# Kernel tuning notes

Hardware: AMD Instinct MI355X
Metric: run time of the kernel (lower is better)

The kernel has to match this reference:

```python
import jax, jax.numpy as jnp
import numpy as np

B, N, D, E = 16, 4096, 1024, 64
TOP_K = 2
ROUTING_FLOOR_BASE = 0.05
CAP_LOW, CAP_HIGH, T_MAX = 0.5, 0.6, 1000


def setup_inputs() -> dict:
    key = jax.random.key(0)
    k1, k2, k3 = jax.random.split(key, 3)
    tokens_B = jax.random.normal(k1, (B, N, D), dtype=jnp.float32)
    t = jax.random.randint(k2, (B,), 0, T_MAX, dtype=jnp.int32)
    W_g = jax.random.normal(k3, (E, D), dtype=jnp.float32) * (1.0 / np.sqrt(D))
    b_g = jnp.zeros((E,), dtype=jnp.float32)
    return {"tokens_B": tokens_B, "t": t, "W_g": W_g, "b_g": b_g}


def _apply_routing_floor(probs, floor):
    # interpolate toward uniform so each expert gets >= floor mass
    e = probs.shape[-1]
    if floor <= 0.0:
        return probs
    alpha = min(floor * e, 1.0)
    return (1.0 - alpha) * probs + alpha / e


def _hard_cap(probs, t):
    # cap(t) = cap_low + (cap_high + cap_low) * t/T_max  (faithful to source)
    t_norm = t.astype(probs.dtype) / T_MAX
    cap = (CAP_LOW + (CAP_HIGH + CAP_LOW) * t_norm)[:, None, None]  # (B,1,1)
    excess = jax.nn.relu(probs - cap)
    capped = probs - excess
    headroom = jax.nn.relu(cap - capped)
    headroom_sum = jnp.clip(headroom.sum(-1, keepdims=True), 1e-8)
    capped = capped + excess.sum(-1, keepdims=True) * (headroom / headroom_sum)
    # torch version runs under no_grad; use straight-through so gate still trains
    return probs + jax.lax.stop_gradient(capped - probs)


def _topk_mask(probs, k):
    vals, idx = jax.lax.top_k(probs, k)  # (B,N,k)
    onehot = jax.nn.one_hot(idx, probs.shape[-1], dtype=probs.dtype)  # (B,N,k,E)
    return jnp.einsum('bnk,bnke->bne', vals, onehot)


def reference(tokens_B, t, W_g, b_g):
    logits = jnp.einsum('bnd,ed->bne', tokens_B, W_g) + b_g  # (B,N,E)
    probs = jax.nn.softmax(logits, axis=-1)
    floor = min(ROUTING_FLOOR_BASE, 0.15 / max(E, 1))
    probs = _apply_routing_floor(probs, floor)
    capped = _hard_cap(probs, t)
    gates = _topk_mask(capped, TOP_K)  # sparse gate mask (B,N,E)
    return gates
```

## Files before the change

### kernel.cpp

```cpp
#include <hip/hip_runtime.h>
#include <hip/hip_bf16.h>

typedef __attribute__((ext_vector_type(8))) short short8;
typedef __attribute__((ext_vector_type(4))) short sh4;
typedef __attribute__((ext_vector_type(4))) float floatx4;

__device__ __forceinline__ bool better(float va, int ia, float vb, int ib) {
    return (va > vb) || (va == vb && ia < ib);
}
__device__ __forceinline__ bool betterd(double va, int ia, double vb, int ib) {
    return (va > vb) || (va == vb && ia < ib);
}

__device__ __forceinline__ short bf16_rn(float f) {
    __hip_bfloat16 h = __float2bfloat16(f);
    return *reinterpret_cast<short*>(&h);
}
__device__ __forceinline__ float bf16_up(short s) {
    return __uint_as_float(((unsigned)(unsigned short)s) << 16);
}

__device__ __forceinline__ void split8(float4 a, float4 b, short8& hi, short8& lo) {
    float v[8] = {a.x, a.y, a.z, a.w, b.x, b.y, b.z, b.w};
    #pragma unroll
    for (int i = 0; i < 8; ++i) {
        short h = bf16_rn(v[i]);
        hi[i] = h;
        lo[i] = bf16_rn(v[i] - bf16_up(h));
    }
}

#define MFMA(A, B, C) __builtin_amdgcn_mfma_f32_16x16x32_bf16((A), (B), (C), 0, 0, 0)

__global__ __launch_bounds__(256)
void wsplit_kernel(const float* __restrict__ Wg,
                   short* __restrict__ whi,
                   short* __restrict__ wlo)
{
    const int i = blockIdx.x * 256 + threadIdx.x;
    float4 v = reinterpret_cast<const float4*>(Wg)[i];
    float vv[4] = {v.x, v.y, v.z, v.w};
    sh4 h, l;
    #pragma unroll
    for (int j = 0; j < 4; ++j) {
        short hh = bf16_rn(vv[j]);
        h[j] = hh;
        l[j] = bf16_rn(vv[j] - bf16_up(hh));
    }
    reinterpret_cast<sh4*>(whi)[i] = h;
    reinterpret_cast<sh4*>(wlo)[i] = l;
}

__global__ __launch_bounds__(256, 4)
void router_kernel(const float* __restrict__ tokens,
                   const int* __restrict__ tarr,
                   const float* __restrict__ bg,
                   float* __restrict__ out,
                   int* __restrict__ flagCount,
                   int* __restrict__ flagList,
                   int listCap,
                   const short* __restrict__ whi,
                   const short* __restrict__ wlo)
{
    __shared__ __align__(16) float gtile[64 * 64];

    const int lane = threadIdx.x & 63;
    const int wave = threadIdx.x >> 6;
    const int c16  = lane & 15;
    const int quad = lane >> 4;

    const int tokenBase = blockIdx.x * 64;
    const int token     = tokenBase + wave * 16 + c16;

    const float4* ap = reinterpret_cast<const float4*>(tokens) + (size_t)token * 256 + quad * 2;
    const short8* whiV = reinterpret_cast<const short8*>(whi);
    const short8* wloV = reinterpret_cast<const short8*>(wlo);
    const int w0 = (c16 +  0) * 128 + quad;
    const int w1 = (c16 + 16) * 128 + quad;
    const int w2 = (c16 + 32) * 128 + quad;
    const int w3 = (c16 + 48) * 128 + quad;

    floatx4 acc0 = {0.f, 0.f, 0.f, 0.f};
    floatx4 acc1 = acc0, acc2 = acc0, acc3 = acc0;

    #pragma unroll
    for (int kb = 0; kb < 32; ++kb) {
        float4 a0 = ap[kb * 8];
        float4 a1 = ap[kb * 8 + 1];
        short8 h0 = whiV[w0 + kb * 4];
        short8 h1 = whiV[w1 + kb * 4];
        short8 h2 = whiV[w2 + kb * 4];
        short8 h3 = whiV[w3 + kb * 4];
        short8 l0 = wloV[w0 + kb * 4];
        short8 l1 = wloV[w1 + kb * 4];
        short8 l2 = wloV[w2 + kb * 4];
        short8 l3 = wloV[w3 + kb * 4];

        short8 ahi, alo;
        split8(a0, a1, ahi, alo);

        acc0 = MFMA(ahi, h0, acc0); acc0 = MFMA(alo, h0, acc0); acc0 = MFMA(ahi, l0, acc0);
        acc1 = MFMA(ahi, h1, acc1); acc1 = MFMA(alo, h1, acc1); acc1 = MFMA(ahi, l1, acc1);
        acc2 = MFMA(ahi, h2, acc2); acc2 = MFMA(alo, h2, acc2); acc2 = MFMA(ahi, l2, acc2);
        acc3 = MFMA(ahi, h3, acc3); acc3 = MFMA(alo, h3, acc3); acc3 = MFMA(ahi, l3, acc3);
    }

    const float b0f = bg[c16 +  0];
    const float b1f = bg[c16 + 16];
    const float b2f = bg[c16 + 32];
    const float b3f = bg[c16 + 48];

    const float tb  = (float)tarr[tokenBase >> 12];
    const float cap = 0.5f + 1.1f * (tb / 1000.0f);

    const float A1 = 0.85f;
    const float A2 = 0.15f / 64.0f;

    #pragma unroll
    for (int r = 0; r < 4; ++r) {
        float l0 = acc0[r] + b0f;
        float l1 = acc1[r] + b1f;
        float l2 = acc2[r] + b2f;
        float l3 = acc3[r] + b3f;

        float mx = fmaxf(fmaxf(l0, l1), fmaxf(l2, l3));
        #pragma unroll
        for (int off = 8; off >= 1; off >>= 1)
            mx = fmaxf(mx, __shfl_xor(mx, off));

        float e0 = expf(l0 - mx), e1 = expf(l1 - mx);
        float e2 = expf(l2 - mx), e3 = expf(l3 - mx);
        float s = e0 + e1 + e2 + e3;
        #pragma unroll
        for (int off = 8; off >= 1; off >>= 1)
            s += __shfl_xor(s, off);
        float inv = 1.0f / s;

        float p0 = A1 * (e0 * inv) + A2;
        float p1 = A1 * (e1 * inv) + A2;
        float p2 = A1 * (e2 * inv) + A2;
        float p3 = A1 * (e3 * inv) + A2;

        float x0 = fmaxf(p0 - cap, 0.f), x1 = fmaxf(p1 - cap, 0.f);
        float x2 = fmaxf(p2 - cap, 0.f), x3 = fmaxf(p3 - cap, 0.f);
        float m0 = p0 - x0, m1 = p1 - x1, m2 = p2 - x2, m3 = p3 - x3;
        float h0 = fmaxf(cap - m0, 0.f), h1 = fmaxf(cap - m1, 0.f);
        float h2 = fmaxf(cap - m2, 0.f), h3 = fmaxf(cap - m3, 0.f);
        float sx = x0 + x1 + x2 + x3;
        float sh = h0 + h1 + h2 + h3;
        #pragma unroll
        for (int off = 8; off >= 1; off >>= 1) {
            sx += __shfl_xor(sx, off);
            sh += __shfl_xor(sh, off);
        }
        sh = fmaxf(sh, 1e-8f);
        float sc = sx / sh;
        float c0 = m0 + sc * h0;
        float c1 = m1 + sc * h1;
        float c2 = m2 + sc * h2;
        float c3 = m3 + sc * h3;

        const int iA = c16, iB = c16 + 16, iC = c16 + 32, iD = c16 + 48;
        float v1, v2; int j1, j2;
        if (better(c0, iA, c1, iB)) { v1 = c0; j1 = iA; v2 = c1; j2 = iB; }
        else                        { v1 = c1; j1 = iB; v2 = c0; j2 = iA; }
        if (better(c2, iC, v1, j1))      { v2 = v1; j2 = j1; v1 = c2; j1 = iC; }
        else if (better(c2, iC, v2, j2)) { v2 = c2; j2 = iC; }
        if (better(c3, iD, v1, j1))      { v2 = v1; j2 = j1; v1 = c3; j1 = iD; }
        else if (better(c3, iD, v2, j2)) { v2 = c3; j2 = iD; }

        #pragma unroll
        for (int off = 1; off < 16; off <<= 1) {
            float w1 = __shfl_xor(v1, off); int k1 = __shfl_xor(j1, off);
            float w2 = __shfl_xor(v2, off); int k2 = __shfl_xor(j2, off);
            if (better(w1, k1, v1, j1)) {
                if (better(v1, j1, w2, k2)) { v2 = v1; j2 = j1; }
                else                        { v2 = w2; j2 = k2; }
                v1 = w1; j1 = k1;
            } else if (better(w1, k1, v2, j2)) {
                v2 = w1; j2 = k1;
            }
        }

        float g0 = (iA == j1 || iA == j2) ? c0 : 0.f;
        float g1 = (iB == j1 || iB == j2) ? c1 : 0.f;
        float g2 = (iC == j1 || iC == j2) ? c2 : 0.f;
        float g3 = (iD == j1 || iD == j2) ? c3 : 0.f;

        float t0 = (iA == j1 || iA == j2) ? -3.0e38f : c0;
        float t1 = (iB == j1 || iB == j2) ? -3.0e38f : c1;
        float t2 = (iC == j1 || iC == j2) ? -3.0e38f : c2;
        float t3 = (iD == j1 || iD == j2) ? -3.0e38f : c3;
        float m3v = fmaxf(fmaxf(t0, t1), fmaxf(t2, t3));
        #pragma unroll
        for (int off = 8; off >= 1; off >>= 1)
            m3v = fmaxf(m3v, __shfl_xor(m3v, off));

        const int tl = wave * 16 + quad * 4 + r;
        bool flag = ((v2 - m3v) < 1e-4f) || (sx > 0.0f);
        if (flag && c16 == 0) {
            int pos = atomicAdd(flagCount, 1);
            if (pos < listCap) flagList[pos] = tokenBase + tl;
        }

        gtile[tl * 64 + iA] = g0;
        gtile[tl * 64 + iB] = g1;
        gtile[tl * 64 + iC] = g2;
        gtile[tl * 64 + iD] = g3;
    }

    __syncthreads();

    const uint4* src = reinterpret_cast<const uint4*>(gtile);
    uint4* dst = reinterpret_cast<uint4*>(out + (size_t)tokenBase * 64);
    dst[threadIdx.x]       = src[threadIdx.x];
    dst[threadIdx.x + 256] = src[threadIdx.x + 256];
    dst[threadIdx.x + 512] = src[threadIdx.x + 512];
    dst[threadIdx.x + 768] = src[threadIdx.x + 768];
}

__global__ __launch_bounds__(256, 4)
void router_kernel_legacy(const float* __restrict__ tokens,
                          const int* __restrict__ tarr,
                          const float* __restrict__ Wg,
                          const float* __restrict__ bg,
                          float* __restrict__ out,
                          int* __restrict__ flagCount,
                          int* __restrict__ flagList,
                          int listCap)
{
    __shared__ __align__(16) float gtile[64 * 64];

    const int lane = threadIdx.x & 63;
    const int wave = threadIdx.x >> 6;
    const int c16  = lane & 15;
    const int quad = lane >> 4;

    const int tokenBase = blockIdx.x * 64;
    const int token     = tokenBase + wave * 16 + c16;

    const float4* ap = reinterpret_cast<const float4*>(tokens) + (size_t)token * 256 + quad * 2;
    const float4* wp0 = reinterpret_cast<const float4*>(Wg) + (size_t)(c16 +  0) * 256 + quad * 2;
    const float4* wp1 = reinterpret_cast<const float4*>(Wg) + (size_t)(c16 + 16) * 256 + quad * 2;
    const float4* wp2 = reinterpret_cast<const float4*>(Wg) + (size_t)(c16 + 32) * 256 + quad * 2;
    const float4* wp3 = reinterpret_cast<const float4*>(Wg) + (size_t)(c16 + 48) * 256 + quad * 2;

    floatx4 acc0 = {0.f, 0.f, 0.f, 0.f};
    floatx4 acc1 = acc0, acc2 = acc0, acc3 = acc0;

    for (int kb = 0; kb < 32; ++kb) {
        short8 ahi, alo;
        split8(ap[kb * 8], ap[kb * 8 + 1], ahi, alo);
        {
            short8 whi, wlo;
            split8(wp0[kb * 8], wp0[kb * 8 + 1], whi, wlo);
            acc0 = MFMA(ahi, whi, acc0);
            acc0 = MFMA(alo, whi, acc0);
            acc0 = MFMA(ahi, wlo, acc0);
        }
        {
            short8 whi, wlo;
            split8(wp1[kb * 8], wp1[kb * 8 + 1], whi, wlo);
            acc1 = MFMA(ahi, whi, acc1);
            acc1 = MFMA(alo, whi, acc1);
            acc1 = MFMA(ahi, wlo, acc1);
        }
        {
            short8 whi, wlo;
            split8(wp2[kb * 8], wp2[kb * 8 + 1], whi, wlo);
            acc2 = MFMA(ahi, whi, acc2);
            acc2 = MFMA(alo, whi, acc2);
            acc2 = MFMA(ahi, wlo, acc2);
        }
        {
            short8 whi, wlo;
            split8(wp3[kb * 8], wp3[kb * 8 + 1], whi, wlo);
            acc3 = MFMA(ahi, whi, acc3);
            acc3 = MFMA(alo, whi, acc3);
            acc3 = MFMA(ahi, wlo, acc3);
        }
    }

    const float b0f = bg[c16 +  0];
    const float b1f = bg[c16 + 16];
    const float b2f = bg[c16 + 32];
    const float b3f = bg[c16 + 48];

    const float tb  = (float)tarr[tokenBase >> 12];
    const float cap = 0.5f + 1.1f * (tb / 1000.0f);

    const float A1 = 0.85f;
    const float A2 = 0.15f / 64.0f;

    #pragma unroll
    for (int r = 0; r < 4; ++r) {
        float l0 = acc0[r] + b0f;
        float l1 = acc1[r] + b1f;
        float l2 = acc2[r] + b2f;
        float l3 = acc3[r] + b3f;

        float mx = fmaxf(fmaxf(l0, l1), fmaxf(l2, l3));
        #pragma unroll
        for (int off = 8; off >= 1; off >>= 1)
            mx = fmaxf(mx, __shfl_xor(mx, off));

        float e0 = expf(l0 - mx), e1 = expf(l1 - mx);
        float e2 = expf(l2 - mx), e3 = expf(l3 - mx);
        float s = e0 + e1 + e2 + e3;
        #pragma unroll
        for (int off = 8; off >= 1; off >>= 1)
            s += __shfl_xor(s, off);
        float inv = 1.0f / s;

        float p0 = A1 * (e0 * inv) + A2;
        float p1 = A1 * (e1 * inv) + A2;
        float p2 = A1 * (e2 * inv) + A2;
        float p3 = A1 * (e3 * inv) + A2;

        float x0 = fmaxf(p0 - cap, 0.f), x1 = fmaxf(p1 - cap, 0.f);
        float x2 = fmaxf(p2 - cap, 0.f), x3 = fmaxf(p3 - cap, 0.f);
        float m0 = p0 - x0, m1 = p1 - x1, m2 = p2 - x2, m3 = p3 - x3;
        float h0 = fmaxf(cap - m0, 0.f), h1 = fmaxf(cap - m1, 0.f);
        float h2 = fmaxf(cap - m2, 0.f), h3 = fmaxf(cap - m3, 0.f);
        float sx = x0 + x1 + x2 + x3;
        float sh = h0 + h1 + h2 + h3;
        #pragma unroll
        for (int off = 8; off >= 1; off >>= 1) {
            sx += __shfl_xor(sx, off);
            sh += __shfl_xor(sh, off);
        }
        sh = fmaxf(sh, 1e-8f);
        float sc = sx / sh;
        float c0 = m0 + sc * h0;
        float c1 = m1 + sc * h1;
        float c2 = m2 + sc * h2;
        float c3 = m3 + sc * h3;

        const int iA = c16, iB = c16 + 16, iC = c16 + 32, iD = c16 + 48;
        float v1, v2; int j1, j2;
        if (better(c0, iA, c1, iB)) { v1 = c0; j1 = iA; v2 = c1; j2 = iB; }
        else                        { v1 = c1; j1 = iB; v2 = c0; j2 = iA; }
        if (better(c2, iC, v1, j1))      { v2 = v1; j2 = j1; v1 = c2; j1 = iC; }
        else if (better(c2, iC, v2, j2)) { v2 = c2; j2 = iC; }
        if (better(c3, iD, v1, j1))      { v2 = v1; j2 = j1; v1 = c3; j1 = iD; }
        else if (better(c3, iD, v2, j2)) { v2 = c3; j2 = iD; }

        #pragma unroll
        for (int off = 1; off < 16; off <<= 1) {
            float w1 = __shfl_xor(v1, off); int k1 = __shfl_xor(j1, off);
            float w2 = __shfl_xor(v2, off); int k2 = __shfl_xor(j2, off);
            if (better(w1, k1, v1, j1)) {
                if (better(v1, j1, w2, k2)) { v2 = v1; j2 = j1; }
                else                        { v2 = w2; j2 = k2; }
                v1 = w1; j1 = k1;
            } else if (better(w1, k1, v2, j2)) {
                v2 = w1; j2 = k1;
            }
        }

        float g0 = (iA == j1 || iA == j2) ? c0 : 0.f;
        float g1 = (iB == j1 || iB == j2) ? c1 : 0.f;
        float g2 = (iC == j1 || iC == j2) ? c2 : 0.f;
        float g3 = (iD == j1 || iD == j2) ? c3 : 0.f;

        float t0 = (iA == j1 || iA == j2) ? -3.0e38f : c0;
        float t1 = (iB == j1 || iB == j2) ? -3.0e38f : c1;
        float t2 = (iC == j1 || iC == j2) ? -3.0e38f : c2;
        float t3 = (iD == j1 || iD == j2) ? -3.0e38f : c3;
        float m3v = fmaxf(fmaxf(t0, t1), fmaxf(t2, t3));
        #pragma unroll
        for (int off = 8; off >= 1; off >>= 1)
            m3v = fmaxf(m3v, __shfl_xor(m3v, off));

        const int tl = wave * 16 + quad * 4 + r;
        bool flag = ((v2 - m3v) < 1e-4f) || (sx > 0.0f);
        if (flag && c16 == 0) {
            int pos = atomicAdd(flagCount, 1);
            if (pos < listCap) flagList[pos] = tokenBase + tl;
        }

        gtile[tl * 64 + iA] = g0;
        gtile[tl * 64 + iB] = g1;
        gtile[tl * 64 + iC] = g2;
        gtile[tl * 64 + iD] = g3;
    }

    __syncthreads();

    const uint4* src = reinterpret_cast<const uint4*>(gtile);
    uint4* dst = reinterpret_cast<uint4*>(out + (size_t)tokenBase * 64);
    dst[threadIdx.x]       = src[threadIdx.x];
    dst[threadIdx.x + 256] = src[threadIdx.x + 256];
    dst[threadIdx.x + 512] = src[threadIdx.x + 512];
    dst[threadIdx.x + 768] = src[threadIdx.x + 768];
}

__global__ __launch_bounds__(256)
void repair_kernel(const float* __restrict__ tokens,
                   const int* __restrict__ tarr,
                   const float* __restrict__ Wg,
                   const float* __restrict__ bg,
                   float* __restrict__ out,
                   const int* __restrict__ cnt,
                   const int* __restrict__ list,
                   int listCap)
{
    __shared__ __align__(16) float atile[8][1024];
    __shared__ double red[256];
    int count = cnt[0];
    if (count > listCap) count = listCap;

    const int e    = threadIdx.x & 63;
    const int part = threadIdx.x >> 6;

    for (int base = blockIdx.x * 8; base < count; base += gridDim.x * 8) {
        const int n = min(8, count - base);

        #pragma unroll
        for (int t = 0; t < 8; ++t) {
            if (t < n) {
                const float4* src =
                    reinterpret_cast<const float4*>(tokens + (size_t)list[base + t] * 1024);
                reinterpret_cast<float4*>(atile[t])[threadIdx.x] = src[threadIdx.x];
            }
        }
        __syncthreads();

        double acc0 = 0.0, acc1 = 0.0, acc2 = 0.0, acc3 = 0.0;
        double acc4 = 0.0, acc5 = 0.0, acc6 = 0.0, acc7 = 0.0;
        const float* wrow = Wg + (size_t)e * 1024 + part * 256;
        const int ko = part * 256;
        for (int k = 0; k < 256; k += 4) {
            float4 wv = *reinterpret_cast<const float4*>(wrow + k);
            const double w0 = (double)wv.x, w1 = (double)wv.y;
            const double w2 = (double)wv.z, w3 = (double)wv.w;
            #define ACC(T, A)                                                   \
                A = fma((double)atile[T][ko + k    ], w0, A);                    \
                A = fma((double)atile[T][ko + k + 1], w1, A);                    \
                A = fma((double)atile[T][ko + k + 2], w2, A);                    \
                A = fma((double)atile[T][ko + k + 3], w3, A);
            ACC(0, acc0) ACC(1, acc1) ACC(2, acc2) ACC(3, acc3)
            ACC(4, acc4) ACC(5, acc5) ACC(6, acc6) ACC(7, acc7)
            #undef ACC
        }

        #pragma unroll
        for (int t = 0; t < 8; ++t) {
            if (t >= n) break;
            double accT = (t == 0) ? acc0 : (t == 1) ? acc1 : (t == 2) ? acc2 :
                          (t == 3) ? acc3 : (t == 4) ? acc4 : (t == 5) ? acc5 :
                          (t == 6) ? acc6 : acc7;
            red[threadIdx.x] = accT;
            __syncthreads();

            if (threadIdx.x < 64) {
                const int token = list[base + t];
                double l = ((red[e] + red[64 + e]) + (red[128 + e] + red[192 + e]))
                         + (double)bg[e];

                double mxv = l;
                #pragma unroll
                for (int off = 32; off >= 1; off >>= 1)
                    mxv = fmax(mxv, __shfl_xor(mxv, off));
                double ex = exp(l - mxv);
                double s = ex;
                #pragma unroll
                for (int off = 32; off >= 1; off >>= 1)
                    s += __shfl_xor(s, off);

                const double alpha = 0.15;
                double p = (1.0 - alpha) * (ex / s) + alpha / 64.0;

                double tb  = (double)tarr[token >> 12];
                double capv = 0.5 + (0.6 + 0.5) * (tb / 1000.0);
                double x = fmax(p - capv, 0.0);
                double m = p - x;
                double h = fmax(capv - m, 0.0);
                double sx = x, sh = h;
                #pragma unroll
                for (int off = 32; off >= 1; off >>= 1) {
                    sx += __shfl_xor(sx, off);
                    sh += __shfl_xor(sh, off);
                }
                sh = fmax(sh, 1e-8);
                double c = m + (sx / sh) * h;

                double v1 = c, v2 = -1.0e300;
                int j1 = e, j2 = 127;
                #pragma unroll
                for (int off = 1; off < 64; off <<= 1) {
                    double w1 = __shfl_xor(v1, off); int k1 = __shfl_xor(j1, off);
                    double w2 = __shfl_xor(v2, off); int k2 = __shfl_xor(j2, off);
                    if (betterd(w1, k1, v1, j1)) {
                        if (betterd(v1, j1, w2, k2)) { v2 = v1; j2 = j1; }
                        else                         { v2 = w2; j2 = k2; }
                        v1 = w1; j1 = k1;
                    } else if (betterd(w1, k1, v2, j2)) {
                        v2 = w1; j2 = k1;
                    }
                }

                float g = (e == j1 || e == j2) ? (float)c : 0.0f;
                out[(size_t)token * 64 + e] = g;
            }
            __syncthreads();
        }
    }
}

extern "C" void kernel_launch(void* const* d_in, const int* in_sizes, int n_in,
                              void* d_out, int out_size, void* d_ws, size_t ws_size,
                              hipStream_t stream) {
    const float* tokens = (const float*)d_in[0];
    const int*   t      = (const int*)d_in[1];
    const float* Wg     = (const float*)d_in[2];
    const float* bg     = (const float*)d_in[3];
    float*       outp   = (float*)d_out;

    int* wsI = (int*)d_ws;
    const long long wsInts = (long long)(ws_size / 4);

    const int  WHALF   = 32768;
    const long long listOff = 16 + 2LL * WHALF;
    long long cap = wsInts - listOff;
    if (cap > 65536) cap = 65536;

    hipMemsetAsync(d_ws, 0, 64, stream);

    if (cap >= 32768) {
        short* whi  = (short*)(wsI + 16);
        short* wlo  = (short*)(wsI + 16 + WHALF);
        int*   list = wsI + listOff;
        wsplit_kernel<<<dim3(64), dim3(256), 0, stream>>>(Wg, whi, wlo);
        router_kernel<<<dim3(65536 / 64), dim3(256), 0, stream>>>(
            tokens, t, bg, outp, wsI, list, (int)cap, whi, wlo);
        repair_kernel<<<dim3(256), dim3(256), 0, stream>>>(
            tokens, t, Wg, bg, outp, wsI, list, (int)cap);
    } else {
        long long cap2 = wsInts - 16;
        if (cap2 < 0) cap2 = 0;
        if (cap2 > 65536) cap2 = 65536;
        router_kernel_legacy<<<dim3(65536 / 64), dim3(256), 0, stream>>>(
            tokens, t, Wg, bg, outp, wsI, wsI + 16, (int)cap2);
        repair_kernel<<<dim3(256), dim3(256), 0, stream>>>(
            tokens, t, Wg, bg, outp, wsI, wsI + 16, (int)cap2);
    }
}
```

Measured before the change: 502.1 us.

## Stage token and weight tiles through double-buffered LDS via async global_load_lds

Replaces the direct per-lane global loads of tokens and split bf16 weights with double-buffered LDS staging filled by global_load_lds. XOR swizzling avoids bank conflicts. The next chunk's load is issued before computing on the current one, with vmcnt waits and barriers between stages. Each block now shares one weight fetch across its four waves instead of each wave loading the full weight set. The cost is 64KB of extra LDS per block, which drops the occupancy target from 4 to 2 blocks per CU and adds barrier synchronisation.

```diff
diff --git a/kernel.cpp b/kernel.cpp
--- a/kernel.cpp
+++ b/kernel.cpp
@@ -31,6 +31,13 @@
 }
 
 #define MFMA(A, B, C) __builtin_amdgcn_mfma_f32_16x16x32_bf16((A), (B), (C), 0, 0, 0)
+
+__device__ __forceinline__ void gload16(const void* g, void* l) {
+    __builtin_amdgcn_global_load_lds(
+        (const __attribute__((address_space(1))) void*)g,
+        (__attribute__((address_space(3))) void*)l,
+        16, 0, 0);
+}
 
 __global__ __launch_bounds__(256)
 void wsplit_kernel(const float* __restrict__ Wg,
@@ -51,7 +58,7 @@
     reinterpret_cast<sh4*>(wlo)[i] = l;
 }
 
-__global__ __launch_bounds__(256, 4)
+__global__ __launch_bounds__(256, 2)
 void router_kernel(const float* __restrict__ tokens,
                    const int* __restrict__ tarr,
                    const float* __restrict__ bg,
@@ -63,6 +70,8 @@
                    const short* __restrict__ wlo)
 {
     __shared__ __align__(16) float gtile[64 * 64];
+    __shared__ __align__(16) char  stage[2][32768];
+    const int A_OFF = 0, WH_OFF = 16384, WL_OFF = 24576;
 
     const int lane = threadIdx.x & 63;
     const int wave = threadIdx.x >> 6;
@@ -70,39 +79,91 @@
     const int quad = lane >> 4;
 
     const int tokenBase = blockIdx.x * 64;
-    const int token     = tokenBase + wave * 16 + c16;
-
-    const float4* ap = reinterpret_cast<const float4*>(tokens) + (size_t)token * 256 + quad * 2;
-    const short8* whiV = reinterpret_cast<const short8*>(whi);
-    const short8* wloV = reinterpret_cast<const short8*>(wlo);
-    const int w0 = (c16 +  0) * 128 + quad;
-    const int w1 = (c16 + 16) * 128 + quad;
-    const int w2 = (c16 + 32) * 128 + quad;
-    const int w3 = (c16 + 48) * 128 + quad;
+
+    const char* tokB = (const char*)tokens;
+    const char* whiB = (const char*)whi;
+    const char* wloB = (const char*)wlo;
+
+    const char* aSrc[4];
+    #pragma unroll
+    for (int j = 0; j < 4; ++j) {
+        const int row = 16 * wave + 4 * j + (lane >> 4);
+        const int v   = ((lane & 15) * 16) ^ ((row & 7) << 4);
+        aSrc[j] = tokB + (size_t)(tokenBase + row) * 4096 + v;
+    }
+    const char* hSrc[2]; const char* lSrc[2];
+    #pragma unroll
+    for (int j = 0; j < 2; ++j) {
+        const int e = 16 * wave + 8 * j + (lane >> 3);
+        const int v = ((lane & 7) * 16) ^ ((e & 7) << 4);
+        hSrc[j] = whiB + (size_t)e * 2048 + v;
+        lSrc[j] = wloB + (size_t)e * 2048 + v;
+    }
 
     floatx4 acc0 = {0.f, 0.f, 0.f, 0.f};
     floatx4 acc1 = acc0, acc2 = acc0, acc3 = acc0;
 
-    #pragma unroll
-    for (int kb = 0; kb < 32; ++kb) {
-        float4 a0 = ap[kb * 8];
-        float4 a1 = ap[kb * 8 + 1];
-        short8 h0 = whiV[w0 + kb * 4];
-        short8 h1 = whiV[w1 + kb * 4];
-        short8 h2 = whiV[w2 + kb * 4];
-        short8 h3 = whiV[w3 + kb * 4];
-        short8 l0 = wloV[w0 + kb * 4];
-        short8 l1 = wloV[w1 + kb * 4];
-        short8 l2 = wloV[w2 + kb * 4];
-        short8 l3 = wloV[w3 + kb * 4];
-
-        short8 ahi, alo;
-        split8(a0, a1, ahi, alo);
-
-        acc0 = MFMA(ahi, h0, acc0); acc0 = MFMA(alo, h0, acc0); acc0 = MFMA(ahi, l0, acc0);
-        acc1 = MFMA(ahi, h1, acc1); acc1 = MFMA(alo, h1, acc1); acc1 = MFMA(ahi, l1, acc1);
-        acc2 = MFMA(ahi, h2, acc2); acc2 = MFMA(alo, h2, acc2); acc2 = MFMA(ahi, l2, acc2);
-        acc3 = MFMA(ahi, h3, acc3); acc3 = MFMA(alo, h3, acc3); acc3 = MFMA(ahi, l3, acc3);
+    const int r  = wave * 16 + c16;
+    const int sw = (c16 & 7) << 4;
+
+    {
+        char* b = stage[0];
+        #pragma unroll
+        for (int j = 0; j < 4; ++j) gload16(aSrc[j], b + A_OFF + (wave * 4 + j) * 1024);
+        #pragma unroll
+        for (int j = 0; j < 2; ++j) gload16(hSrc[j], b + WH_OFF + (wave * 2 + j) * 1024);
+        #pragma unroll
+        for (int j = 0; j < 2; ++j) gload16(lSrc[j], b + WL_OFF + (wave * 2 + j) * 1024);
+    }
+
+    int p = 0;
+    for (int c = 0; c < 16; ++c) {
+        if (c < 15) {
+            char* b = stage[p ^ 1];
+            const int co = (c + 1) * 256;
+            const int cw = (c + 1) * 128;
+            #pragma unroll
+            for (int j = 0; j < 4; ++j) gload16(aSrc[j] + co, b + A_OFF + (wave * 4 + j) * 1024);
+            #pragma unroll
+            for (int j = 0; j < 2; ++j) gload16(hSrc[j] + cw, b + WH_OFF + (wave * 2 + j) * 1024);
+            #pragma unroll
+            for (int j = 0; j < 2; ++j) gload16(lSrc[j] + cw, b + WL_OFF + (wave * 2 + j) * 1024);
+            asm volatile("s_waitcnt vmcnt(8)" ::: "memory");
+        } else {
+            asm volatile("s_waitcnt vmcnt(0)" ::: "memory");
+        }
+        __builtin_amdgcn_s_barrier();
+        asm volatile("" ::: "memory");
+
+        const char* bA = stage[p] + A_OFF;
+        const char* bH = stage[p] + WH_OFF;
+        const char* bL = stage[p] + WL_OFF;
+        #pragma unroll
+        for (int kb = 0; kb < 2; ++kb) {
+            float4 a0 = *(const float4*)(bA + r * 256 + ((kb * 128 + quad * 32 +  0) ^ sw));
+            float4 a1 = *(const float4*)(bA + r * 256 + ((kb * 128 + quad * 32 + 16) ^ sw));
+            const int wu = (kb * 64 + quad * 16) ^ sw;
+            short8 h0 = *(const short8*)(bH + (c16 +  0) * 128 + wu);
+            short8 h1 = *(const short8*)(bH + (c16 + 16) * 128 + wu);
+            short8 h2 = *(const short8*)(bH + (c16 + 32) * 128 + wu);
+            short8 h3 = *(const short8*)(bH + (c16 + 48) * 128 + wu);
+            short8 l0 = *(const short8*)(bL + (c16 +  0) * 128 + wu);
+            short8 l1 = *(const short8*)(bL + (c16 + 16) * 128 + wu);
+            short8 l2 = *(const short8*)(bL + (c16 + 32) * 128 + wu);
+            short8 l3 = *(const short8*)(bL + (c16 + 48) * 128 + wu);
+
+            short8 ahi, alo;
+            split8(a0, a1, ahi, alo);
+
+            acc0 = MFMA(ahi, h0, acc0); acc0 = MFMA(alo, h0, acc0); acc0 = MFMA(ahi, l0, acc0);
+            acc1 = MFMA(ahi, h1, acc1); acc1 = MFMA(alo, h1, acc1); acc1 = MFMA(ahi, l1, acc1);
+            acc2 = MFMA(ahi, h2, acc2); acc2 = MFMA(alo, h2, acc2); acc2 = MFMA(ahi, l2, acc2);
+            acc3 = MFMA(ahi, h3, acc3); acc3 = MFMA(alo, h3, acc3); acc3 = MFMA(ahi, l3, acc3);
+        }
+
+        __builtin_amdgcn_s_barrier();
+        asm volatile("" ::: "memory");
+        p ^= 1;
     }
 
     const float b0f = bg[c16 +  0];
@@ -117,11 +178,11 @@
     const float A2 = 0.15f / 64.0f;
 
     #pragma unroll
-    for (int r = 0; r < 4; ++r) {
-        float l0 = acc0[r] + b0f;
-        float l1 = acc1[r] + b1f;
-        float l2 = acc2[r] + b2f;
-        float l3 = acc3[r] + b3f;
+    for (int rr = 0; rr < 4; ++rr) {
+        float l0 = acc0[rr] + b0f;
+        float l1 = acc1[rr] + b1f;
+        float l2 = acc2[rr] + b2f;
+        float l3 = acc3[rr] + b3f;
 
         float mx = fmaxf(fmaxf(l0, l1), fmaxf(l2, l3));
         #pragma unroll
@@ -196,7 +257,7 @@
         for (int off = 8; off >= 1; off >>= 1)
             m3v = fmaxf(m3v, __shfl_xor(m3v, off));
 
-        const int tl = wave * 16 + quad * 4 + r;
+        const int tl = wave * 16 + quad * 4 + rr;
         bool flag = ((v2 - m3v) < 1e-4f) || (sx > 0.0f);
         if (flag && c16 == 0) {
             int pos = atomicAdd(flagCount, 1);
```

Result: faster. 445.3 us (-11.3%).

## Double-buffer token and weight chunks into LDS via async global_load_lds

Applied to the files above, without the earlier changes.

Restructures the router GEMM main loop into a double-buffered pipeline. Each iteration issues global_load_lds for the next K-chunk of tokens and pre-split bf16 weights while computing on the current chunk, with waitcnt and barriers between stages. The weight split kernel now writes weights in an MFMA-fragment-ordered layout so each wave can copy contiguous 16-byte lanes straight into LDS. The aim is to hide global load latency and cut redundant per-wave weight fetches. In exchange it adds two barriers per iteration and a larger LDS footprint, which may lower occupancy.

```diff
diff --git a/kernel.cpp b/kernel.cpp
--- a/kernel.cpp
+++ b/kernel.cpp
@@ -32,23 +32,30 @@
 
 #define MFMA(A, B, C) __builtin_amdgcn_mfma_f32_16x16x32_bf16((A), (B), (C), 0, 0, 0)
 
+__device__ __forceinline__ void gload16(const void* g, void* l) {
+    __builtin_amdgcn_global_load_lds(
+        (const __attribute__((address_space(1))) void*)g,
+        (__attribute__((address_space(3))) void*)l,
+        16, 0, 0);
+}
+
 __global__ __launch_bounds__(256)
 void wsplit_kernel(const float* __restrict__ Wg,
                    short* __restrict__ whi,
                    short* __restrict__ wlo)
 {
-    const int i = blockIdx.x * 256 + threadIdx.x;
-    float4 v = reinterpret_cast<const float4*>(Wg)[i];
-    float vv[4] = {v.x, v.y, v.z, v.w};
-    sh4 h, l;
-    #pragma unroll
-    for (int j = 0; j < 4; ++j) {
-        short hh = bf16_rn(vv[j]);
-        h[j] = hh;
-        l[j] = bf16_rn(vv[j] - bf16_up(hh));
-    }
-    reinterpret_cast<sh4*>(whi)[i] = h;
-    reinterpret_cast<sh4*>(wlo)[i] = l;
+    const int idx = blockIdx.x * 256 + threadIdx.x;
+    const int c = idx >> 8;
+    const int g = (idx >> 6) & 3;
+    const int q = (idx >> 4) & 3;
+    const int e = idx & 15;
+    const float* src = Wg + (size_t)(g * 16 + e) * 1024 + c * 32 + q * 8;
+    float4 v0 = reinterpret_cast<const float4*>(src)[0];
+    float4 v1 = reinterpret_cast<const float4*>(src)[1];
+    short8 hi, lo;
+    split8(v0, v1, hi, lo);
+    reinterpret_cast<short8*>(whi)[idx] = hi;
+    reinterpret_cast<short8*>(wlo)[idx] = lo;
 }
 
 __global__ __launch_bounds__(256, 4)
@@ -62,7 +69,8 @@
                    const short* __restrict__ whi,
                    const short* __restrict__ wlo)
 {
-    __shared__ __align__(16) float gtile[64 * 64];
+    __shared__ __align__(16) char smem[32768];
+    const int WH_OFF = 8192, WL_OFF = 12288;
 
     const int lane = threadIdx.x & 63;
     const int wave = threadIdx.x >> 6;
@@ -70,31 +78,54 @@
     const int quad = lane >> 4;
 
     const int tokenBase = blockIdx.x * 64;
-    const int token     = tokenBase + wave * 16 + c16;
-
-    const float4* ap = reinterpret_cast<const float4*>(tokens) + (size_t)token * 256 + quad * 2;
-    const short8* whiV = reinterpret_cast<const short8*>(whi);
-    const short8* wloV = reinterpret_cast<const short8*>(wlo);
-    const int w0 = (c16 +  0) * 128 + quad;
-    const int w1 = (c16 + 16) * 128 + quad;
-    const int w2 = (c16 + 32) * 128 + quad;
-    const int w3 = (c16 + 48) * 128 + quad;
+
+    const char* aS0 = (const char*)tokens
+        + (size_t)(tokenBase + wave * 16 + c16) * 4096 + quad * 32;
+    const char* hS = (const char*)whi + wave * 1024 + (size_t)lane * 16;
+    const char* lS = (const char*)wlo + wave * 1024 + (size_t)lane * 16;
 
     floatx4 acc0 = {0.f, 0.f, 0.f, 0.f};
     floatx4 acc1 = acc0, acc2 = acc0, acc3 = acc0;
 
-    #pragma unroll
-    for (int kb = 0; kb < 32; ++kb) {
-        float4 a0 = ap[kb * 8];
-        float4 a1 = ap[kb * 8 + 1];
-        short8 h0 = whiV[w0 + kb * 4];
-        short8 h1 = whiV[w1 + kb * 4];
-        short8 h2 = whiV[w2 + kb * 4];
-        short8 h3 = whiV[w3 + kb * 4];
-        short8 l0 = wloV[w0 + kb * 4];
-        short8 l1 = wloV[w1 + kb * 4];
-        short8 l2 = wloV[w2 + kb * 4];
-        short8 l3 = wloV[w3 + kb * 4];
+    const int aRd = wave * 2048 + lane * 16;
+    const int wRd = lane * 16;
+
+    {
+        char* b = smem;
+        gload16(aS0,      b + wave * 2048);
+        gload16(aS0 + 16, b + wave * 2048 + 1024);
+        gload16(hS, b + WH_OFF + wave * 1024);
+        gload16(lS, b + WL_OFF + wave * 1024);
+    }
+
+    for (int c = 0; c < 32; ++c) {
+        char* cur = smem + (c & 1) * 16384;
+        char* nxt = smem + ((c & 1) ^ 1) * 16384;
+
+        if (c < 31) {
+            const int co = (c + 1) * 128;
+            const int cw = (c + 1) * 4096;
+            gload16(aS0 + co,      nxt + wave * 2048);
+            gload16(aS0 + co + 16, nxt + wave * 2048 + 1024);
+            gload16(hS + cw, nxt + WH_OFF + wave * 1024);
+            gload16(lS + cw, nxt + WL_OFF + wave * 1024);
+            asm volatile("s_waitcnt vmcnt(4)" ::: "memory");
+        } else {
+            asm volatile("s_waitcnt vmcnt(0)" ::: "memory");
+        }
+        __builtin_amdgcn_s_barrier();
+        asm volatile("" ::: "memory");
+
+        float4 a0 = *(const float4*)(cur + aRd);
+        float4 a1 = *(const float4*)(cur + aRd + 1024);
+        short8 h0 = *(const short8*)(cur + WH_OFF +    0 + wRd);
+        short8 h1 = *(const short8*)(cur + WH_OFF + 1024 + wRd);
+        short8 h2 = *(const short8*)(cur + WH_OFF + 2048 + wRd);
+        short8 h3 = *(const short8*)(cur + WH_OFF + 3072 + wRd);
+        short8 l0 = *(const short8*)(cur + WL_OFF +    0 + wRd);
+        short8 l1 = *(const short8*)(cur + WL_OFF + 1024 + wRd);
+        short8 l2 = *(const short8*)(cur + WL_OFF + 2048 + wRd);
+        short8 l3 = *(const short8*)(cur + WL_OFF + 3072 + wRd);
 
         short8 ahi, alo;
         split8(a0, a1, ahi, alo);
@@ -103,7 +134,14 @@
         acc1 = MFMA(ahi, h1, acc1); acc1 = MFMA(alo, h1, acc1); acc1 = MFMA(ahi, l1, acc1);
         acc2 = MFMA(ahi, h2, acc2); acc2 = MFMA(alo, h2, acc2); acc2 = MFMA(ahi, l2, acc2);
         acc3 = MFMA(ahi, h3, acc3); acc3 = MFMA(alo, h3, acc3); acc3 = MFMA(ahi, l3, acc3);
-    }
+
+        __builtin_amdgcn_s_barrier();
+        asm volatile("" ::: "memory");
+    }
+
+    __syncthreads();
+
+    float* gtile = reinterpret_cast<float*>(smem);
 
     const float b0f = bg[c16 +  0];
     const float b1f = bg[c16 + 16];
@@ -117,11 +155,11 @@
     const float A2 = 0.15f / 64.0f;
 
     #pragma unroll
-    for (int r = 0; r < 4; ++r) {
-        float l0 = acc0[r] + b0f;
-        float l1 = acc1[r] + b1f;
-        float l2 = acc2[r] + b2f;
-        float l3 = acc3[r] + b3f;
+    for (int rr = 0; rr < 4; ++rr) {
+        float l0 = acc0[rr] + b0f;
+        float l1 = acc1[rr] + b1f;
+        float l2 = acc2[rr] + b2f;
+        float l3 = acc3[rr] + b3f;
 
         float mx = fmaxf(fmaxf(l0, l1), fmaxf(l2, l3));
         #pragma unroll
@@ -196,7 +234,7 @@
         for (int off = 8; off >= 1; off >>= 1)
             m3v = fmaxf(m3v, __shfl_xor(m3v, off));
 
-        const int tl = wave * 16 + quad * 4 + r;
+        const int tl = wave * 16 + quad * 4 + rr;
         bool flag = ((v2 - m3v) < 1e-4f) || (sx > 0.0f);
         if (flag && c16 == 0) {
             int pos = atomicAdd(flagCount, 1);
@@ -531,7 +569,7 @@
         short* whi  = (short*)(wsI + 16);
         short* wlo  = (short*)(wsI + 16 + WHALF);
         int*   list = wsI + listOff;
-        wsplit_kernel<<<dim3(64), dim3(256), 0, stream>>>(Wg, whi, wlo);
+        wsplit_kernel<<<dim3(32), dim3(256), 0, stream>>>(Wg, whi, wlo);
         router_kernel<<<dim3(65536 / 64), dim3(256), 0, stream>>>(
             tokens, t, bg, outp, wsI, list, (int)cap, whi, wlo);
         repair_kernel<<<dim3(256), dim3(256), 0, stream>>>(
```

New measurement: 448.4 us. 10.7% less time.
